# Kernel tuning notes

Hardware: AMD Instinct MI355X
Metric: run time of the kernel (lower is better)

Reference implementation:

```python
import jax, jax.numpy as jnp
import numpy as np

IN_SIZE = 171
HIDDEN = 1024
OUT_SIZE = 171
BATCH = 64
SEQ_LEN = 100
COND_NUM = 5
GT_NUM = 5


def _lstm_cell(x, h, c, w_ih, w_hh, b_ih, b_hh):
    # PyTorch LSTMCell: gates ordered (i, f, g, o)
    gates = x @ w_ih.T + h @ w_hh.T + b_ih + b_hh  # [B, 4H]
    i, f, g, o = jnp.split(gates, 4, axis=-1)
    i = jax.nn.sigmoid(i)
    f = jax.nn.sigmoid(f)
    g = jnp.tanh(g)
    o = jax.nn.sigmoid(o)
    c_new = f * c + i * g
    h_new = o * jnp.tanh(c_new)
    return h_new, c_new


def setup_inputs() -> dict:
    key = jax.random.key(0)
    ks = jax.random.split(key, 15)
    s = 1.0 / np.sqrt(HIDDEN)
    p = {}
    p["real_seq"] = jax.random.normal(ks[0], (BATCH, SEQ_LEN, IN_SIZE), dtype=jnp.float32)
    p["w_ih1"] = jax.random.uniform(ks[1], (4 * HIDDEN, IN_SIZE), minval=-s, maxval=s, dtype=jnp.float32)
    p["w_hh1"] = jax.random.uniform(ks[2], (4 * HIDDEN, HIDDEN), minval=-s, maxval=s, dtype=jnp.float32)
    p["b_ih1"] = jax.random.uniform(ks[3], (4 * HIDDEN,), minval=-s, maxval=s, dtype=jnp.float32)
    p["b_hh1"] = jax.random.uniform(ks[4], (4 * HIDDEN,), minval=-s, maxval=s, dtype=jnp.float32)
    p["w_ih2"] = jax.random.uniform(ks[5], (4 * HIDDEN, HIDDEN), minval=-s, maxval=s, dtype=jnp.float32)
    p["w_hh2"] = jax.random.uniform(ks[6], (4 * HIDDEN, HIDDEN), minval=-s, maxval=s, dtype=jnp.float32)
    p["b_ih2"] = jax.random.uniform(ks[7], (4 * HIDDEN,), minval=-s, maxval=s, dtype=jnp.float32)
    p["b_hh2"] = jax.random.uniform(ks[8], (4 * HIDDEN,), minval=-s, maxval=s, dtype=jnp.float32)
    p["w_ih3"] = jax.random.uniform(ks[9], (4 * HIDDEN, HIDDEN), minval=-s, maxval=s, dtype=jnp.float32)
    p["w_hh3"] = jax.random.uniform(ks[10], (4 * HIDDEN, HIDDEN), minval=-s, maxval=s, dtype=jnp.float32)
    p["b_ih3"] = jax.random.uniform(ks[11], (4 * HIDDEN,), minval=-s, maxval=s, dtype=jnp.float32)
    p["b_hh3"] = jax.random.uniform(ks[12], (4 * HIDDEN,), minval=-s, maxval=s, dtype=jnp.float32)
    p["dec_w"] = jax.random.uniform(ks[13], (OUT_SIZE, HIDDEN), minval=-s, maxval=s, dtype=jnp.float32)
    p["dec_b"] = jax.random.uniform(ks[14], (OUT_SIZE,), minval=-s, maxval=s, dtype=jnp.float32)
    return p


def _condition_lst(seq_len):
    gt = np.ones((100, GT_NUM))
    cond = np.zeros((100, COND_NUM))
    return np.concatenate((gt, cond), axis=1).reshape(-1)[:seq_len]


def reference(real_seq, w_ih1, w_hh1, b_ih1, b_hh1, w_ih2, w_hh2, b_ih2, b_hh2,
              w_ih3, w_hh3, b_ih3, b_hh3, dec_w, dec_b):
    batch, seq_len, _ = real_seq.shape
    cond = jnp.asarray(_condition_lst(seq_len), dtype=real_seq.dtype)  # [T], static pattern
    frames = jnp.swapaxes(real_seq, 0, 1)  # [T, B, in]
    z = jnp.zeros((batch, HIDDEN), dtype=real_seq.dtype)
    out0 = jnp.zeros((batch, OUT_SIZE), dtype=real_seq.dtype)

    def step(carry, xs):
        (h0, c0, h1, c1, h2, c2, prev_out) = carry
        frame, c = xs
        in_frame = jnp.where(c == 1, frame, prev_out)
        h0, c0 = _lstm_cell(in_frame, h0, c0, w_ih1, w_hh1, b_ih1, b_hh1)
        h1, c1 = _lstm_cell(h0, h1, c1, w_ih2, w_hh2, b_ih2, b_hh2)
        h2, c2 = _lstm_cell(h1, h2, c2, w_ih3, w_hh3, b_ih3, b_hh3)
        out = h2 @ dec_w.T + dec_b
        return (h0, c0, h1, c1, h2, c2, out), out

    _, outs = jax.lax.scan(step, (z, z, z, z, z, z, out0), (frames, cond))  # outs [T, B, out]
    # torch concatenates along dim=1 -> [B, T*out]
    return jnp.swapaxes(outs, 0, 1).reshape(batch, seq_len * OUT_SIZE)
```

## Files before the change

### kernel.cpp

```cpp
#include <hip/hip_runtime.h>
#include <hip/hip_fp16.h>


typedef unsigned short u16;
typedef unsigned int u32;
typedef _Float16 f16;
typedef _Float16 h8 __attribute__((ext_vector_type(8)));
typedef float f4 __attribute__((ext_vector_type(4)));
typedef u32 u32x4 __attribute__((ext_vector_type(4)));
typedef u32 u32x2 __attribute__((ext_vector_type(2)));

#define HSZ 65536
#define SENT 0xFFFFFFFFu

static __device__ __forceinline__ f4 mfma16(h8 a, h8 b, f4 c) {
  return __builtin_amdgcn_mfma_f32_16x16x32_f16(a, b, c, 0, 0, 0);
}

static __device__ __forceinline__ float fsig(float x) {
  return 1.f / (1.f + __expf(-x));
}
static __device__ __forceinline__ float ftanh(float x) {
  return 1.f - 2.f / (1.f + __expf(2.f * x));
}

static __device__ __forceinline__ u32 sentmax(h8 v) {
  union { h8 h; u32x4 u; } cv; cv.h = v;
  u32 a = cv.u.x > cv.u.y ? cv.u.x : cv.u.y;
  u32 b = cv.u.z > cv.u.w ? cv.u.z : cv.u.w;
  return a > b ? a : b;
}

static __device__ __forceinline__ h8 bypass_load(const u16* p) {
  u32x4 v;
  asm volatile("global_load_dwordx4 %0, %1, off sc0 sc1"
               : "=v"(v) : "v"(p) : "memory");
  union { u32x4 u; h8 h; } cv; cv.u = v;
  return cv.h;
}

static __device__ __forceinline__ void vm_drain_fence() {
  __builtin_amdgcn_s_waitcnt(0x0f70);
  __builtin_amdgcn_sched_barrier(0);
}

struct P {
  const u16 *w1h, *weff, *w1x, *w2, *w3, *wdec, *fr;
  const float *br, *ba, *b2s, *b3s, *dec_b;
  u16 *h0, *h1, *h2;
  float* out;
};

template<int NJ>
static __device__ __forceinline__ void gemm_hreg(f4* acc, const u16* __restrict__ h,
                                                 const h8 (&wr)[NJ], int kq, int bt2,
                                                 int q, int c) {
  h8 a[NJ * 2];
#pragma unroll
  for (int jj = 0; jj < NJ; ++jj) {
    const u16* hp = h + (size_t)((kq * 8 + jj) * 4 + q) * 512;
#pragma unroll
    for (int t = 0; t < 2; ++t)
      a[jj * 2 + t] = *(const h8*)(hp + ((bt2 * 2 + t) * 16 + c) * 8);
  }
  u32 mx = 0;
#pragma unroll
  for (int i = 0; i < NJ * 2; ++i) { u32 s = sentmax(a[i]); mx = mx > s ? mx : s; }
  if (__builtin_expect(__any((int)(mx == SENT)), 0)) {
    for (;;) {
#pragma unroll
      for (int jj = 0; jj < NJ; ++jj) {
        const u16* hp = h + (size_t)((kq * 8 + jj) * 4 + q) * 512;
#pragma unroll
        for (int t = 0; t < 2; ++t)
          a[jj * 2 + t] = bypass_load(hp + ((bt2 * 2 + t) * 16 + c) * 8);
      }
      vm_drain_fence();
      mx = 0;
#pragma unroll
      for (int i = 0; i < NJ * 2; ++i) { u32 s = sentmax(a[i]); mx = mx > s ? mx : s; }
      if (!__any((int)(mx == SENT))) break;
    }
  }
#pragma unroll
  for (int jj = 0; jj < NJ; ++jj)
#pragma unroll
    for (int t = 0; t < 2; ++t)
      acc[t] = mfma16(a[jj * 2 + t], wr[jj], acc[t]);
}

static __device__ __forceinline__ void gemm_hlds(f4* acc, const u16* __restrict__ h,
                                                 const u16* lw, int ktbase, int kq,
                                                 int bt2, int q, int c, int lane) {
  h8 a[16];
#pragma unroll
  for (int jj = 0; jj < 8; ++jj) {
    const u16* hp = h + (size_t)((kq * 8 + jj) * 4 + q) * 512;
#pragma unroll
    for (int t = 0; t < 2; ++t)
      a[jj * 2 + t] = *(const h8*)(hp + ((bt2 * 2 + t) * 16 + c) * 8);
  }
  u32 mx = 0;
#pragma unroll
  for (int i = 0; i < 16; ++i) { u32 s = sentmax(a[i]); mx = mx > s ? mx : s; }
  if (__builtin_expect(__any((int)(mx == SENT)), 0)) {
    for (;;) {
#pragma unroll
      for (int jj = 0; jj < 8; ++jj) {
        const u16* hp = h + (size_t)((kq * 8 + jj) * 4 + q) * 512;
#pragma unroll
        for (int t = 0; t < 2; ++t)
          a[jj * 2 + t] = bypass_load(hp + ((bt2 * 2 + t) * 16 + c) * 8);
      }
      vm_drain_fence();
      mx = 0;
#pragma unroll
      for (int i = 0; i < 16; ++i) { u32 s = sentmax(a[i]); mx = mx > s ? mx : s; }
      if (!__any((int)(mx == SENT))) break;
    }
  }
#pragma unroll
  for (int jj = 0; jj < 8; ++jj) {
    h8 b = *(const h8*)(lw + (size_t)((ktbase + kq * 8 + jj) * 64 + lane) * 8);
    acc[0] = mfma16(a[jj * 2 + 0], b, acc[0]);
    acc[1] = mfma16(a[jj * 2 + 1], b, acc[1]);
  }
}

static __device__ __forceinline__ void gemm_fr(f4* acc, const u16* __restrict__ frt,
                                               const h8 (&wr)[2], int kq, int bt2,
                                               int q, int c) {
  if (kq < 3) {
#pragma unroll
    for (int jj = 0; jj < 2; ++jj) {
      int kt = kq * 2 + jj;
      h8 b = wr[jj];
#pragma unroll
      for (int t = 0; t < 2; ++t) {
        h8 a = *(const h8*)(frt + (size_t)((bt2 * 2 + t) * 16 + c) * 192 + kt * 32 + q * 8);
        acc[t] = mfma16(a, b, acc[t]);
      }
    }
  }
}

__launch_bounds__(512, 2)
__global__ void lstm_main(P p) {
  const int ng = blockIdx.x;
  const int tid = threadIdx.x;
  const int lane = tid & 63;
  const int w = tid >> 6;
  const int kq = w & 3;
  const int bt2 = w >> 2;
  const int c = lane & 15;
  const int q = lane >> 4;

  __shared__ u16 lds_w2[64 * 512];
  __shared__ u16 lds_w3[64 * 512];
  __shared__ float part[4 * 64 * 17];
  __shared__ float decp[8][64];

  {
    const uint4* s2 = (const uint4*)(p.w2 + (size_t)ng * 64 * 512);
    const uint4* s3 = (const uint4*)(p.w3 + (size_t)ng * 64 * 512);
    uint4* d2 = (uint4*)lds_w2;
    uint4* d3 = (uint4*)lds_w3;
    for (int i = tid; i < 4096; i += 512) { d2[i] = s2[i]; d3[i] = s3[i]; }
  }

  h8 r_w1h[8], r_weff[8], r_w1x[2];
  {
#pragma unroll
    for (int jj = 0; jj < 8; ++jj) {
      r_w1h[jj] = *(const h8*)(p.w1h + (size_t)((ng * 32 + kq * 8 + jj) * 64 + lane) * 8);
      r_weff[jj] = *(const h8*)(p.weff + (size_t)((ng * 32 + kq * 8 + jj) * 64 + lane) * 8);
    }
    if (kq < 3) {
#pragma unroll
      for (int jj = 0; jj < 2; ++jj)
        r_w1x[jj] = *(const h8*)(p.w1x + (size_t)((ng * 6 + kq * 2 + jj) * 64 + lane) * 8);
    }
  }

  float rb_r[16], rb_a[16], rb2[16], rb3[16];
  if (w == 0) {
#pragma unroll
    for (int i = 0; i < 16; ++i) {
      int idx = (i >> 2) * 1024 + ng * 4 + (i & 3);
      rb_r[i] = p.br[idx];  rb_a[i] = p.ba[idx];
      rb2[i] = p.b2s[idx];  rb3[i] = p.b3s[idx];
    }
  }
  const float dec_bng = (ng < 171) ? p.dec_b[ng] : 0.f;
  __syncthreads();

  float cr0[4] = {0, 0, 0, 0}, cr1[4] = {0, 0, 0, 0}, cr2[4] = {0, 0, 0, 0};

  auto combine_pub = [&](float* crL, const float* rb, u16* hw) {
    __builtin_amdgcn_s_setprio(1);
    u32 pk0 = 0, pk1 = 0;
#pragma unroll
    for (int u = 0; u < 4; ++u) {
      float s0 = rb[0 + u], s1 = rb[4 + u], s2 = rb[8 + u], s3 = rb[12 + u];
#pragma unroll
      for (int kqi = 0; kqi < 4; ++kqi) {
        const float* pp = &part[(kqi * 64 + lane) * 17 + u];
        s0 += pp[0]; s1 += pp[4]; s2 += pp[8]; s3 += pp[12];
      }
      float iv = fsig(s0), fv = fsig(s1), gv = ftanh(s2), ov = fsig(s3);
      float cn = fv * crL[u] + iv * gv;
      crL[u] = cn;
      f16 hh = (f16)(ov * ftanh(cn));
      u32 bits = (u32)*(const u16*)&hh;
      if (u < 2) pk0 |= bits << (16 * u); else pk1 |= bits << (16 * (u - 2));
    }
    u32* dst = (u32*)hw + (size_t)(ng >> 1) * 256 + lane * 4 + (ng & 1) * 2;
    u32x2 pk; pk.x = pk0; pk.y = pk1;
    asm volatile("global_store_dwordx2 %0, %1, off sc0 sc1"
                 : : "v"(dst), "v"(pk) : "memory");
    __builtin_amdgcn_s_setprio(0);
  };

  auto canary_wait = [&](const u16* slot) {
    if (w == 1) {
      const u32* cp = (const u32*)slot + (size_t)lane * 512;
      for (;;) {
        u32x4 v0, v1;
        asm volatile("global_load_dwordx4 %0, %2, off sc0 sc1\n\t"
                     "global_load_dwordx4 %1, %3, off sc0 sc1"
                     : "=v"(v0), "=v"(v1) : "v"(cp), "v"(cp + 256) : "memory");
        vm_drain_fence();
        u32 a0 = v0.x > v0.y ? v0.x : v0.y;
        u32 a1 = v0.z > v0.w ? v0.z : v0.w;
        u32 a2 = v1.x > v1.y ? v1.x : v1.y;
        u32 a3 = v1.z > v1.w ? v1.z : v1.w;
        u32 m01 = a0 > a1 ? a0 : a1;
        u32 m23 = a2 > a3 ? a2 : a3;
        u32 m = m01 > m23 ? m01 : m23;
        if (__all((int)(m != SENT))) break;
      }
    }
    __syncthreads();
  };

  auto put_part = [&](const f4* acc) {
#pragma unroll
    for (int t = 0; t < 2; ++t)
#pragma unroll
      for (int r = 0; r < 4; ++r)
        part[(kq * 64 + bt2 * 32 + t * 16 + q * 4 + r) * 17 + c] = acc[t][r];
  };

  auto dec_partial = [&](const u16* __restrict__ h2b) {
    if (ng < 171) {
      const u16* hp = h2b + (size_t)w * 16 * 512 + lane * 8;
      const u16* wp = p.wdec + (size_t)ng * 1024 + w * 128;
      h8 hv[16];
#pragma unroll
      for (int i = 0; i < 16; ++i) hv[i] = *(const h8*)(hp + (size_t)i * 512);
      u32 mx = 0;
#pragma unroll
      for (int i = 0; i < 16; ++i) { u32 s = sentmax(hv[i]); mx = mx > s ? mx : s; }
      if (__builtin_expect(__any((int)(mx == SENT)), 0)) {
        for (;;) {
#pragma unroll
          for (int i = 0; i < 16; ++i) hv[i] = bypass_load(hp + (size_t)i * 512);
          vm_drain_fence();
          mx = 0;
#pragma unroll
          for (int i = 0; i < 16; ++i) { u32 s = sentmax(hv[i]); mx = mx > s ? mx : s; }
          if (!__any((int)(mx == SENT))) break;
        }
      }
      float s = 0.f;
#pragma unroll
      for (int i = 0; i < 16; ++i) {
        h8 wv8 = *(const h8*)(wp + i * 8);
#pragma unroll
        for (int jj = 0; jj < 8; ++jj) s += (float)hv[i][jj] * (float)wv8[jj];
      }
      decp[w][lane] = s;
    }
  };
  auto dec_reduce = [&](int tout) {
    if (ng < 171) {
      float o = dec_bng;
#pragma unroll
      for (int i = 0; i < 8; ++i) o += decp[i][lane];
      p.out[(size_t)lane * 17100 + (size_t)tout * 171 + ng] = o;
    }
  };

  for (int t = 0; t < 100; ++t) {
    const bool cond = (t % 10) < 5;
    const bool hoisted = cond && (t > 0);
    const u16* h0r = p.h0 + (size_t)t * HSZ;
    const u16* h1r = p.h1 + (size_t)t * HSZ;
    const u16* h2r = p.h2 + (size_t)t * HSZ;
    u16* h0w = p.h0 + (size_t)(t + 1) * HSZ;
    u16* h1w = p.h1 + (size_t)(t + 1) * HSZ;
    u16* h2w = p.h2 + (size_t)(t + 1) * HSZ;

    if (!hoisted) {
      f4 acc[2] = {{0, 0, 0, 0}, {0, 0, 0, 0}};
      gemm_hreg<8>(acc, h0r, r_w1h, kq, bt2, q, c);
      if (cond) {
        gemm_fr(acc, p.fr + (size_t)t * 64 * 192, r_w1x, kq, bt2, q, c);
        __syncthreads();
      } else {
        canary_wait(h2r);
        gemm_hreg<8>(acc, h2r, r_weff, kq, bt2, q, c);
      }
      put_part(acc);
      __syncthreads();
      if (w == 0) combine_pub(cr0, cond ? rb_r : rb_a, h0w);
    }
    {
      f4 acc[2] = {{0, 0, 0, 0}, {0, 0, 0, 0}};
      gemm_hlds(acc, h1r, lds_w2, 32, kq, bt2, q, c, lane);
      canary_wait(h0w);
      gemm_hlds(acc, h0w, lds_w2, 0, kq, bt2, q, c, lane);
      put_part(acc);
      __syncthreads();
      if (w == 0) combine_pub(cr1, rb2, h1w);
      if ((t + 1 < 100) && (((t + 1) % 10) < 5)) {
        f4 accA[2] = {{0, 0, 0, 0}, {0, 0, 0, 0}};
        gemm_hreg<8>(accA, h0w, r_w1h, kq, bt2, q, c);
        gemm_fr(accA, p.fr + (size_t)(t + 1) * 64 * 192, r_w1x, kq, bt2, q, c);
        __syncthreads();
        put_part(accA);
        __syncthreads();
        if (w == 0) combine_pub(cr0, rb_r, p.h0 + (size_t)(t + 2) * HSZ);
      }
    }
    {
      f4 acc[2] = {{0, 0, 0, 0}, {0, 0, 0, 0}};
      gemm_hlds(acc, h2r, lds_w3, 32, kq, bt2, q, c, lane);
      if (t > 0) dec_partial(h2r);
      canary_wait(h1w);
      gemm_hlds(acc, h1w, lds_w3, 0, kq, bt2, q, c, lane);
      put_part(acc);
      __syncthreads();
      if (w == 0) combine_pub(cr2, rb3, h2w);
      else if (w == 1 && t > 0) dec_reduce(t - 1);
    }
  }
  canary_wait(p.h2 + (size_t)100 * HSZ);
  dec_partial(p.h2 + (size_t)100 * HSZ);
  __syncthreads();
  if (w == 0) dec_reduce(99);
}


__global__ void pack_w_kernel(const float* __restrict__ srcA, int KA,
                              const float* __restrict__ srcB, int KB,
                              u16* __restrict__ dst, int nkt) {
  int blk = blockIdx.x;
  int ng = blk / nkt, kt = blk % nkt;
  int lane = threadIdx.x;
  int c = lane & 15, q = lane >> 4;
  int row = (c >> 2) * 1024 + ng * 4 + (c & 3);
  int k0 = kt * 32 + q * 8;
  alignas(16) u16 outv[8];
  for (int j = 0; j < 8; ++j) {
    int k = k0 + j;
    float v = 0.f;
    if (k < KA) v = srcA[(size_t)row * KA + k];
    else if (k - KA < KB) v = srcB[(size_t)row * KB + (k - KA)];
    f16 hv = (f16)v;
    outv[j] = *(u16*)&hv;
  }
  *(uint4*)(dst + ((size_t)blk * 64 + lane) * 8) = *(const uint4*)outv;
}

__global__ void pack_weff_kernel(const float* __restrict__ w_ih1,
                                 const float* __restrict__ dec_w, u16* __restrict__ dst) {
  int blk = blockIdx.x;
  int ng = blk >> 5, kt = blk & 31;
  int lane = threadIdx.x;
  int c = lane & 15, q = lane >> 4;
  int row = (c >> 2) * 1024 + ng * 4 + (c & 3);
  int k0 = kt * 32 + q * 8;
  float acc[8] = {0.f, 0.f, 0.f, 0.f, 0.f, 0.f, 0.f, 0.f};
  for (int r = 0; r < 171; ++r) {
    float wi = w_ih1[(size_t)row * 171 + r];
    const float* dw = dec_w + (size_t)r * 1024 + k0;
#pragma unroll
    for (int j = 0; j < 8; ++j) acc[j] += wi * dw[j];
  }
  alignas(16) u16 outv[8];
  for (int j = 0; j < 8; ++j) { f16 hv = (f16)acc[j]; outv[j] = *(u16*)&hv; }
  *(uint4*)(dst + ((size_t)blk * 64 + lane) * 8) = *(const uint4*)outv;
}

__global__ void prep_bias_kernel(const float* b_ih1, const float* b_hh1,
                                 const float* w_ih1, const float* dec_b,
                                 const float* b_ih2, const float* b_hh2,
                                 const float* b_ih3, const float* b_hh3,
                                 float* br, float* ba, float* b2, float* b3) {
  int n = blockIdx.x * 256 + threadIdx.x;
  float s = b_ih1[n] + b_hh1[n];
  br[n] = s;
  float a = 0.f;
  for (int r = 0; r < 171; ++r) a += w_ih1[(size_t)n * 171 + r] * dec_b[r];
  ba[n] = s + a;
  b2[n] = b_ih2[n] + b_hh2[n];
  b3[n] = b_ih3[n] + b_hh3[n];
}

__global__ void pack_frames_kernel(const float* __restrict__ rs, u16* __restrict__ fr) {
  int i = blockIdx.x * 256 + threadIdx.x;
  int j = i % 192;
  int tb = i / 192;
  int b = tb % 64, t = tb / 64;
  float v = (j < 171) ? rs[((size_t)b * 100 + t) * 171 + j] : 0.f;
  f16 hv = (f16)v;
  fr[i] = *(u16*)&hv;
}

__global__ void pack_wdec_kernel(const float* __restrict__ dw, u16* __restrict__ dst) {
  int i = blockIdx.x * 256 + threadIdx.x;
  if (i < 171 * 1024) { f16 hv = (f16)dw[i]; dst[i] = *(u16*)&hv; }
}

__global__ void init_kernel(u32* h0, u32* h1, u32* h2) {
  int i = blockIdx.x * 256 + threadIdx.x;
  const int SLOT = 32768;
  u32 v = (i < SLOT) ? 0u : SENT;
  h0[i] = v; h1[i] = v; h2[i] = v;
}

extern "C" void kernel_launch(void* const* d_in, const int* in_sizes, int n_in,
                              void* d_out, int out_size, void* d_ws, size_t ws_size,
                              hipStream_t stream) {
  const float* real_seq = (const float*)d_in[0];
  const float* w_ih1 = (const float*)d_in[1];
  const float* w_hh1 = (const float*)d_in[2];
  const float* b_ih1 = (const float*)d_in[3];
  const float* b_hh1 = (const float*)d_in[4];
  const float* w_ih2 = (const float*)d_in[5];
  const float* w_hh2 = (const float*)d_in[6];
  const float* b_ih2 = (const float*)d_in[7];
  const float* b_hh2 = (const float*)d_in[8];
  const float* w_ih3 = (const float*)d_in[9];
  const float* w_hh3 = (const float*)d_in[10];
  const float* b_ih3 = (const float*)d_in[11];
  const float* b_hh3 = (const float*)d_in[12];
  const float* dec_w = (const float*)d_in[13];
  const float* dec_b = (const float*)d_in[14];

  char* ws = (char*)d_ws;
  size_t off = 0;
  auto alloc = [&](size_t bytes) {
    char* pp = ws + off;
    off += (bytes + 255) & ~(size_t)255;
    return pp;
  };
  u16* w1h  = (u16*)alloc(256ULL * 32 * 512 * 2);
  u16* weff = (u16*)alloc(256ULL * 32 * 512 * 2);
  u16* w1x  = (u16*)alloc(256ULL * 6 * 512 * 2);
  u16* w2   = (u16*)alloc(256ULL * 64 * 512 * 2);
  u16* w3   = (u16*)alloc(256ULL * 64 * 512 * 2);
  u16* wdec = (u16*)alloc(171ULL * 1024 * 2);
  u16* fr   = (u16*)alloc(100ULL * 64 * 192 * 2);
  u16* h0   = (u16*)alloc(101ULL * HSZ * 2);
  u16* h1   = (u16*)alloc(101ULL * HSZ * 2);
  u16* h2   = (u16*)alloc(101ULL * HSZ * 2);
  float* br  = (float*)alloc(4096 * 4);
  float* ba  = (float*)alloc(4096 * 4);
  float* b2s = (float*)alloc(4096 * 4);
  float* b3s = (float*)alloc(4096 * 4);
  (void)ws_size; (void)in_sizes; (void)n_in; (void)out_size;

  pack_w_kernel<<<256 * 32, 64, 0, stream>>>(w_hh1, 1024, nullptr, 0, w1h, 32);
  pack_w_kernel<<<256 * 6, 64, 0, stream>>>(w_ih1, 171, nullptr, 0, w1x, 6);
  pack_w_kernel<<<256 * 64, 64, 0, stream>>>(w_ih2, 1024, w_hh2, 1024, w2, 64);
  pack_w_kernel<<<256 * 64, 64, 0, stream>>>(w_ih3, 1024, w_hh3, 1024, w3, 64);
  pack_weff_kernel<<<256 * 32, 64, 0, stream>>>(w_ih1, dec_w, weff);
  pack_wdec_kernel<<<(171 * 1024 + 255) / 256, 256, 0, stream>>>(dec_w, wdec);
  pack_frames_kernel<<<100 * 64 * 192 / 256, 256, 0, stream>>>(real_seq, fr);
  prep_bias_kernel<<<16, 256, 0, stream>>>(b_ih1, b_hh1, w_ih1, dec_b,
                                           b_ih2, b_hh2, b_ih3, b_hh3, br, ba, b2s, b3s);
  init_kernel<<<101 * 32768 / 256, 256, 0, stream>>>((u32*)h0, (u32*)h1, (u32*)h2);

  P p{w1h, weff, w1x, w2, w3, wdec, fr, br, ba, b2s, b3s, dec_b,
      h0, h1, h2, (float*)d_out};
  lstm_main<<<256, 512, 0, stream>>>(p);
}
```

Baseline: 1.689 ms.

## Replace single-wave canary polling with per-wave prefetched canary checks

The old wait had one wave poll the sentinel values of the incoming hidden state and then release the block with a barrier. Now every wave issues its own canary load for just the slice it will consume before starting the independent GEMM half, then checks it afterwards. The poll latency is hidden behind compute and the barrier is removed from the dependency wait path. It adds a barrier before put_part, and correctness now depends on each wave's canary slice fully covering the data that wave reads.

```diff
diff --git a/kernel.cpp b/kernel.cpp
--- a/kernel.cpp
+++ b/kernel.cpp
@@ -37,6 +37,13 @@
                : "=v"(v) : "v"(p) : "memory");
   union { u32x4 u; h8 h; } cv; cv.u = v;
   return cv.h;
+}
+
+static __device__ __forceinline__ u32x2 bypass_load8(const u32* p) {
+  u32x2 v;
+  asm volatile("global_load_dwordx2 %0, %1, off sc0 sc1"
+               : "=v"(v) : "v"(p) : "memory");
+  return v;
 }
 
 static __device__ __forceinline__ void vm_drain_fence() {
@@ -221,26 +228,20 @@
     __builtin_amdgcn_s_setprio(0);
   };
 
-  auto canary_wait = [&](const u16* slot) {
-    if (w == 1) {
-      const u32* cp = (const u32*)slot + (size_t)lane * 512;
-      for (;;) {
-        u32x4 v0, v1;
-        asm volatile("global_load_dwordx4 %0, %2, off sc0 sc1\n\t"
-                     "global_load_dwordx4 %1, %3, off sc0 sc1"
-                     : "=v"(v0), "=v"(v1) : "v"(cp), "v"(cp + 256) : "memory");
-        vm_drain_fence();
-        u32 a0 = v0.x > v0.y ? v0.x : v0.y;
-        u32 a1 = v0.z > v0.w ? v0.z : v0.w;
-        u32 a2 = v1.x > v1.y ? v1.x : v1.y;
-        u32 a3 = v1.z > v1.w ? v1.z : v1.w;
-        u32 m01 = a0 > a1 ? a0 : a1;
-        u32 m23 = a2 > a3 ? a2 : a3;
-        u32 m = m01 > m23 ? m01 : m23;
-        if (__all((int)(m != SENT))) break;
-      }
-    }
-    __syncthreads();
+  auto canq_issue = [&](const u16* slot) -> u32x2 {
+    const u32* cp = (const u32*)slot +
+                    (size_t)(kq * 32 + (lane >> 1)) * 256 + (lane & 1) * 2;
+    return bypass_load8(cp);
+  };
+  auto canq_wait = [&](const u16* slot, u32x2 v) {
+    const u32* cp = (const u32*)slot +
+                    (size_t)(kq * 32 + (lane >> 1)) * 256 + (lane & 1) * 2;
+    for (;;) {
+      u32 m = v.x > v.y ? v.x : v.y;
+      if (__all((int)(m != SENT))) break;
+      v = bypass_load8(cp);
+      vm_drain_fence();
+    }
   };
 
   auto put_part = [&](const f4* acc) {
@@ -288,6 +289,17 @@
 #pragma unroll
       for (int i = 0; i < 8; ++i) o += decp[i][lane];
       p.out[(size_t)lane * 17100 + (size_t)tout * 171 + ng] = o;
+    }
+  };
+
+  auto dec_wait = [&](const u16* slot) {
+    const u32* cp = (const u32*)slot +
+                    (size_t)(w * 16 + (lane & 15)) * 256 + ((lane >> 4) & 1) * 2;
+    for (;;) {
+      u32x2 v = bypass_load8(cp);
+      vm_drain_fence();
+      u32 m = v.x > v.y ? v.x : v.y;
+      if (__all((int)(m != SENT))) break;
     }
   };
 
@@ -303,23 +315,32 @@
 
     if (!hoisted) {
       f4 acc[2] = {{0, 0, 0, 0}, {0, 0, 0, 0}};
-      gemm_hreg<8>(acc, h0r, r_w1h, kq, bt2, q, c);
       if (cond) {
+        gemm_hreg<8>(acc, h0r, r_w1h, kq, bt2, q, c);
         gemm_fr(acc, p.fr + (size_t)t * 64 * 192, r_w1x, kq, bt2, q, c);
-        __syncthreads();
       } else {
-        canary_wait(h2r);
+        u32x2 cv = canq_issue(h2r);
+        gemm_hreg<8>(acc, h0r, r_w1h, kq, bt2, q, c);
+        vm_drain_fence();
+        canq_wait(h2r, cv);
         gemm_hreg<8>(acc, h2r, r_weff, kq, bt2, q, c);
       }
+      __syncthreads();
       put_part(acc);
       __syncthreads();
       if (w == 0) combine_pub(cr0, cond ? rb_r : rb_a, h0w);
     }
     {
       f4 acc[2] = {{0, 0, 0, 0}, {0, 0, 0, 0}};
+      u32x2 cv = {0, 0};
+      if (!hoisted) cv = canq_issue(h0w);
       gemm_hlds(acc, h1r, lds_w2, 32, kq, bt2, q, c, lane);
-      canary_wait(h0w);
+      if (!hoisted) {
+        vm_drain_fence();
+        canq_wait(h0w, cv);
+      }
       gemm_hlds(acc, h0w, lds_w2, 0, kq, bt2, q, c, lane);
+      __syncthreads();
       put_part(acc);
       __syncthreads();
       if (w == 0) combine_pub(cr1, rb2, h1w);
@@ -335,17 +356,20 @@
     }
     {
       f4 acc[2] = {{0, 0, 0, 0}, {0, 0, 0, 0}};
+      u32x2 cv = canq_issue(h1w);
       gemm_hlds(acc, h2r, lds_w3, 32, kq, bt2, q, c, lane);
       if (t > 0) dec_partial(h2r);
-      canary_wait(h1w);
+      vm_drain_fence();
+      canq_wait(h1w, cv);
       gemm_hlds(acc, h1w, lds_w3, 0, kq, bt2, q, c, lane);
+      __syncthreads();
       put_part(acc);
       __syncthreads();
       if (w == 0) combine_pub(cr2, rb3, h2w);
       else if (w == 1 && t > 0) dec_reduce(t - 1);
     }
   }
-  canary_wait(p.h2 + (size_t)100 * HSZ);
+  dec_wait(p.h2 + (size_t)100 * HSZ);
   dec_partial(p.h2 + (size_t)100 * HSZ);
   __syncthreads();
   if (w == 0) dec_reduce(99);
```

Measured after the change: 1.860 ms. +10.1%, slower.

## Split LSTM gate combine across two waves and prefetch canary polls before GEMMs

Applied to the files above, without the earlier changes.

The gate-combine/publish step that wave 0 used to do alone over 4 hidden units is now shared by waves 0 and 1, two units each, with one dword store apiece. This shortens the serial tail on the critical path between layers. The readiness (canary) poll moves to wave 7 and is split into issue and finish phases. The first load is issued before the independent half of the GEMM so its latency overlaps the compute, and the decoder reduce moves to wave 2. The cost is more waves in the combine phase and extra registers held across the GEMMs for the prefetched values.

```diff
diff --git a/kernel.cpp b/kernel.cpp
--- a/kernel.cpp
+++ b/kernel.cpp
@@ -182,11 +182,11 @@
     }
   }
 
-  float rb_r[16], rb_a[16], rb2[16], rb3[16];
-  if (w == 0) {
-#pragma unroll
-    for (int i = 0; i < 16; ++i) {
-      int idx = (i >> 2) * 1024 + ng * 4 + (i & 3);
+  float rb_r[8], rb_a[8], rb2[8], rb3[8];
+  if (w < 2) {
+#pragma unroll
+    for (int i = 0; i < 8; ++i) {
+      int idx = (i >> 1) * 1024 + ng * 4 + w * 2 + (i & 1);
       rb_r[i] = p.br[idx];  rb_a[i] = p.ba[idx];
       rb2[i] = p.b2s[idx];  rb3[i] = p.b3s[idx];
     }
@@ -194,41 +194,44 @@
   const float dec_bng = (ng < 171) ? p.dec_b[ng] : 0.f;
   __syncthreads();
 
-  float cr0[4] = {0, 0, 0, 0}, cr1[4] = {0, 0, 0, 0}, cr2[4] = {0, 0, 0, 0};
+  float cr0[2] = {0, 0}, cr1[2] = {0, 0}, cr2[2] = {0, 0};
 
   auto combine_pub = [&](float* crL, const float* rb, u16* hw) {
     __builtin_amdgcn_s_setprio(1);
-    u32 pk0 = 0, pk1 = 0;
-#pragma unroll
-    for (int u = 0; u < 4; ++u) {
-      float s0 = rb[0 + u], s1 = rb[4 + u], s2 = rb[8 + u], s3 = rb[12 + u];
+    u32 pk = 0;
+#pragma unroll
+    for (int lu = 0; lu < 2; ++lu) {
+      int u = (w << 1) + lu;
+      float s0 = rb[0 + lu], s1 = rb[2 + lu], s2 = rb[4 + lu], s3 = rb[6 + lu];
 #pragma unroll
       for (int kqi = 0; kqi < 4; ++kqi) {
         const float* pp = &part[(kqi * 64 + lane) * 17 + u];
         s0 += pp[0]; s1 += pp[4]; s2 += pp[8]; s3 += pp[12];
       }
       float iv = fsig(s0), fv = fsig(s1), gv = ftanh(s2), ov = fsig(s3);
-      float cn = fv * crL[u] + iv * gv;
-      crL[u] = cn;
+      float cn = fv * crL[lu] + iv * gv;
+      crL[lu] = cn;
       f16 hh = (f16)(ov * ftanh(cn));
-      u32 bits = (u32)*(const u16*)&hh;
-      if (u < 2) pk0 |= bits << (16 * u); else pk1 |= bits << (16 * (u - 2));
-    }
-    u32* dst = (u32*)hw + (size_t)(ng >> 1) * 256 + lane * 4 + (ng & 1) * 2;
-    u32x2 pk; pk.x = pk0; pk.y = pk1;
-    asm volatile("global_store_dwordx2 %0, %1, off sc0 sc1"
+      pk |= ((u32)*(const u16*)&hh) << (16 * lu);
+    }
+    u32* dst = (u32*)hw + (size_t)(ng >> 1) * 256 + lane * 4 + (ng & 1) * 2 + w;
+    asm volatile("global_store_dword %0, %1, off sc0 sc1"
                  : : "v"(dst), "v"(pk) : "memory");
     __builtin_amdgcn_s_setprio(0);
   };
 
-  auto canary_wait = [&](const u16* slot) {
-    if (w == 1) {
+  auto can_issue = [&](const u16* slot, u32x4* v0, u32x4* v1) {
+    if (w == 7) {
+      const u32* cp = (const u32*)slot + (size_t)lane * 512;
+      asm volatile("global_load_dwordx4 %0, %2, off sc0 sc1\n\t"
+                   "global_load_dwordx4 %1, %3, off sc0 sc1"
+                   : "=v"(*v0), "=v"(*v1) : "v"(cp), "v"(cp + 256) : "memory");
+    }
+  };
+  auto can_finish = [&](const u16* slot, u32x4 v0, u32x4 v1) {
+    if (w == 7) {
       const u32* cp = (const u32*)slot + (size_t)lane * 512;
       for (;;) {
-        u32x4 v0, v1;
-        asm volatile("global_load_dwordx4 %0, %2, off sc0 sc1\n\t"
-                     "global_load_dwordx4 %1, %3, off sc0 sc1"
-                     : "=v"(v0), "=v"(v1) : "v"(cp), "v"(cp + 256) : "memory");
         vm_drain_fence();
         u32 a0 = v0.x > v0.y ? v0.x : v0.y;
         u32 a1 = v0.z > v0.w ? v0.z : v0.w;
@@ -238,6 +241,9 @@
         u32 m23 = a2 > a3 ? a2 : a3;
         u32 m = m01 > m23 ? m01 : m23;
         if (__all((int)(m != SENT))) break;
+        asm volatile("global_load_dwordx4 %0, %2, off sc0 sc1\n\t"
+                     "global_load_dwordx4 %1, %3, off sc0 sc1"
+                     : "=v"(v0), "=v"(v1) : "v"(cp), "v"(cp + 256) : "memory");
       }
     }
     __syncthreads();
@@ -303,26 +309,31 @@
 
     if (!hoisted) {
       f4 acc[2] = {{0, 0, 0, 0}, {0, 0, 0, 0}};
-      gemm_hreg<8>(acc, h0r, r_w1h, kq, bt2, q, c);
       if (cond) {
+        gemm_hreg<8>(acc, h0r, r_w1h, kq, bt2, q, c);
         gemm_fr(acc, p.fr + (size_t)t * 64 * 192, r_w1x, kq, bt2, q, c);
         __syncthreads();
       } else {
-        canary_wait(h2r);
+        u32x4 cv0 = {0, 0, 0, 0}, cv1 = {0, 0, 0, 0};
+        can_issue(h2r, &cv0, &cv1);
+        gemm_hreg<8>(acc, h0r, r_w1h, kq, bt2, q, c);
+        can_finish(h2r, cv0, cv1);
         gemm_hreg<8>(acc, h2r, r_weff, kq, bt2, q, c);
       }
       put_part(acc);
       __syncthreads();
-      if (w == 0) combine_pub(cr0, cond ? rb_r : rb_a, h0w);
+      if (w < 2) combine_pub(cr0, cond ? rb_r : rb_a, h0w);
     }
     {
       f4 acc[2] = {{0, 0, 0, 0}, {0, 0, 0, 0}};
+      u32x4 cv0 = {0, 0, 0, 0}, cv1 = {0, 0, 0, 0};
+      can_issue(h0w, &cv0, &cv1);
       gemm_hlds(acc, h1r, lds_w2, 32, kq, bt2, q, c, lane);
-      canary_wait(h0w);
+      can_finish(h0w, cv0, cv1);
       gemm_hlds(acc, h0w, lds_w2, 0, kq, bt2, q, c, lane);
       put_part(acc);
       __syncthreads();
-      if (w == 0) combine_pub(cr1, rb2, h1w);
+      if (w < 2) combine_pub(cr1, rb2, h1w);
       if ((t + 1 < 100) && (((t + 1) % 10) < 5)) {
         f4 accA[2] = {{0, 0, 0, 0}, {0, 0, 0, 0}};
         gemm_hreg<8>(accA, h0w, r_w1h, kq, bt2, q, c);
@@ -330,25 +341,31 @@
         __syncthreads();
         put_part(accA);
         __syncthreads();
-        if (w == 0) combine_pub(cr0, rb_r, p.h0 + (size_t)(t + 2) * HSZ);
+        if (w < 2) combine_pub(cr0, rb_r, p.h0 + (size_t)(t + 2) * HSZ);
       }
     }
     {
       f4 acc[2] = {{0, 0, 0, 0}, {0, 0, 0, 0}};
+      u32x4 cv0 = {0, 0, 0, 0}, cv1 = {0, 0, 0, 0};
+      can_issue(h1w, &cv0, &cv1);
       gemm_hlds(acc, h2r, lds_w3, 32, kq, bt2, q, c, lane);
       if (t > 0) dec_partial(h2r);
-      canary_wait(h1w);
+      can_finish(h1w, cv0, cv1);
       gemm_hlds(acc, h1w, lds_w3, 0, kq, bt2, q, c, lane);
       put_part(acc);
       __syncthreads();
-      if (w == 0) combine_pub(cr2, rb3, h2w);
-      else if (w == 1 && t > 0) dec_reduce(t - 1);
-    }
-  }
-  canary_wait(p.h2 + (size_t)100 * HSZ);
-  dec_partial(p.h2 + (size_t)100 * HSZ);
-  __syncthreads();
-  if (w == 0) dec_reduce(99);
+      if (w < 2) combine_pub(cr2, rb3, h2w);
+      else if (w == 2 && t > 0) dec_reduce(t - 1);
+    }
+  }
+  {
+    u32x4 cv0 = {0, 0, 0, 0}, cv1 = {0, 0, 0, 0};
+    can_issue(p.h2 + (size_t)100 * HSZ, &cv0, &cv1);
+    can_finish(p.h2 + (size_t)100 * HSZ, cv0, cv1);
+    dec_partial(p.h2 + (size_t)100 * HSZ);
+    __syncthreads();
+    if (w == 0) dec_reduce(99);
+  }
 }
 
 
```

Measured after the change: 1.825 ms. 8.0% more time.

## Replace sentinel canary polling with per-step flag arrays and early flag prefetch

Applied to the files above, without the earlier changes.

Inter-block readiness is now signalled through a dedicated array of per-block flags, one per publish sequence, instead of polling the hidden-state buffers for sentinel values. Each publishing wave writes its flag after its h store. The waiting wave issues the flag load before the preceding independent GEMM, so the poll latency can overlap useful work. This shrinks polling traffic to one 16-byte load per lane and removes the max-reduction over data. The cost is that readiness no longer checks the data itself: lane 0's flag store is not explicitly ordered after the other lanes' data stores, which could let a consumer read stale h.

```diff
diff --git a/kernel.cpp b/kernel.cpp
--- a/kernel.cpp
+++ b/kernel.cpp
@@ -12,6 +12,7 @@
 
 #define HSZ 65536
 #define SENT 0xFFFFFFFFu
+#define NSEQ 320
 
 static __device__ __forceinline__ f4 mfma16(h8 a, h8 b, f4 c) {
   return __builtin_amdgcn_mfma_f32_16x16x32_f16(a, b, c, 0, 0, 0);
@@ -48,6 +49,7 @@
   const u16 *w1h, *weff, *w1x, *w2, *w3, *wdec, *fr;
   const float *br, *ba, *b2s, *b3s, *dec_b;
   u16 *h0, *h1, *h2;
+  u32* flg;
   float* out;
 };
 
@@ -196,7 +198,7 @@
 
   float cr0[4] = {0, 0, 0, 0}, cr1[4] = {0, 0, 0, 0}, cr2[4] = {0, 0, 0, 0};
 
-  auto combine_pub = [&](float* crL, const float* rb, u16* hw) {
+  auto combine_pub = [&](float* crL, const float* rb, u16* hw, int seqv) {
     __builtin_amdgcn_s_setprio(1);
     u32 pk0 = 0, pk1 = 0;
 #pragma unroll
@@ -218,26 +220,33 @@
     u32x2 pk; pk.x = pk0; pk.y = pk1;
     asm volatile("global_store_dwordx2 %0, %1, off sc0 sc1"
                  : : "v"(dst), "v"(pk) : "memory");
+    if (lane == 0) {
+      u32* fp = p.flg + (size_t)seqv * 256 + ng;
+      u32 one = 1;
+      asm volatile("global_store_dword %0, %1, off sc0 sc1"
+                   : : "v"(fp), "v"(one) : "memory");
+    }
     __builtin_amdgcn_s_setprio(0);
   };
 
-  auto canary_wait = [&](const u16* slot) {
+  auto flag_issue = [&](int seqv, u32x4* v) {
     if (w == 1) {
-      const u32* cp = (const u32*)slot + (size_t)lane * 512;
+      const u32* fp = p.flg + (size_t)seqv * 256 + lane * 4;
+      asm volatile("global_load_dwordx4 %0, %1, off sc0 sc1"
+                   : "=v"(*v) : "v"(fp) : "memory");
+    }
+  };
+  auto flag_finish = [&](int seqv, u32x4 v) {
+    if (w == 1) {
+      const u32* fp = p.flg + (size_t)seqv * 256 + lane * 4;
       for (;;) {
-        u32x4 v0, v1;
-        asm volatile("global_load_dwordx4 %0, %2, off sc0 sc1\n\t"
-                     "global_load_dwordx4 %1, %3, off sc0 sc1"
-                     : "=v"(v0), "=v"(v1) : "v"(cp), "v"(cp + 256) : "memory");
         vm_drain_fence();
-        u32 a0 = v0.x > v0.y ? v0.x : v0.y;
-        u32 a1 = v0.z > v0.w ? v0.z : v0.w;
-        u32 a2 = v1.x > v1.y ? v1.x : v1.y;
-        u32 a3 = v1.z > v1.w ? v1.z : v1.w;
-        u32 m01 = a0 > a1 ? a0 : a1;
-        u32 m23 = a2 > a3 ? a2 : a3;
-        u32 m = m01 > m23 ? m01 : m23;
-        if (__all((int)(m != SENT))) break;
+        u32 m01 = v.x < v.y ? v.x : v.y;
+        u32 m23 = v.z < v.w ? v.z : v.w;
+        u32 mn = m01 < m23 ? m01 : m23;
+        if (__all((int)(mn != 0))) break;
+        asm volatile("global_load_dwordx4 %0, %1, off sc0 sc1"
+                     : "=v"(v) : "v"(fp) : "memory");
       }
     }
     __syncthreads();
@@ -291,9 +300,12 @@
     }
   };
 
+  int seq = 0, seqA = 0, seqB = 0, seqC = 0;
+
   for (int t = 0; t < 100; ++t) {
     const bool cond = (t % 10) < 5;
     const bool hoisted = cond && (t > 0);
+    const bool hoistNext = (t + 1 < 100) && (((t + 1) % 10) < 5);
     const u16* h0r = p.h0 + (size_t)t * HSZ;
     const u16* h1r = p.h1 + (size_t)t * HSZ;
     const u16* h2r = p.h2 + (size_t)t * HSZ;
@@ -303,52 +315,67 @@
 
     if (!hoisted) {
       f4 acc[2] = {{0, 0, 0, 0}, {0, 0, 0, 0}};
-      gemm_hreg<8>(acc, h0r, r_w1h, kq, bt2, q, c);
       if (cond) {
+        gemm_hreg<8>(acc, h0r, r_w1h, kq, bt2, q, c);
         gemm_fr(acc, p.fr + (size_t)t * 64 * 192, r_w1x, kq, bt2, q, c);
         __syncthreads();
       } else {
-        canary_wait(h2r);
+        u32x4 fv = {0, 0, 0, 0};
+        flag_issue(seqC, &fv);
+        gemm_hreg<8>(acc, h0r, r_w1h, kq, bt2, q, c);
+        flag_finish(seqC, fv);
         gemm_hreg<8>(acc, h2r, r_weff, kq, bt2, q, c);
       }
       put_part(acc);
       __syncthreads();
-      if (w == 0) combine_pub(cr0, cond ? rb_r : rb_a, h0w);
+      seqA = seq++;
+      if (w == 0) combine_pub(cr0, cond ? rb_r : rb_a, h0w, seqA);
     }
     {
       f4 acc[2] = {{0, 0, 0, 0}, {0, 0, 0, 0}};
+      u32x4 fv = {0, 0, 0, 0};
+      flag_issue(seqA, &fv);
       gemm_hlds(acc, h1r, lds_w2, 32, kq, bt2, q, c, lane);
-      canary_wait(h0w);
+      flag_finish(seqA, fv);
       gemm_hlds(acc, h0w, lds_w2, 0, kq, bt2, q, c, lane);
       put_part(acc);
       __syncthreads();
-      if (w == 0) combine_pub(cr1, rb2, h1w);
-      if ((t + 1 < 100) && (((t + 1) % 10) < 5)) {
+      seqB = seq++;
+      if (w == 0) combine_pub(cr1, rb2, h1w, seqB);
+      if (hoistNext) {
         f4 accA[2] = {{0, 0, 0, 0}, {0, 0, 0, 0}};
         gemm_hreg<8>(accA, h0w, r_w1h, kq, bt2, q, c);
         gemm_fr(accA, p.fr + (size_t)(t + 1) * 64 * 192, r_w1x, kq, bt2, q, c);
         __syncthreads();
         put_part(accA);
         __syncthreads();
-        if (w == 0) combine_pub(cr0, rb_r, p.h0 + (size_t)(t + 2) * HSZ);
+        seqA = seq++;
+        if (w == 0) combine_pub(cr0, rb_r, p.h0 + (size_t)(t + 2) * HSZ, seqA);
       }
     }
     {
       f4 acc[2] = {{0, 0, 0, 0}, {0, 0, 0, 0}};
+      u32x4 fv = {0, 0, 0, 0};
+      flag_issue(seqB, &fv);
       gemm_hlds(acc, h2r, lds_w3, 32, kq, bt2, q, c, lane);
       if (t > 0) dec_partial(h2r);
-      canary_wait(h1w);
+      flag_finish(seqB, fv);
       gemm_hlds(acc, h1w, lds_w3, 0, kq, bt2, q, c, lane);
       put_part(acc);
       __syncthreads();
-      if (w == 0) combine_pub(cr2, rb3, h2w);
+      seqC = seq++;
+      if (w == 0) combine_pub(cr2, rb3, h2w, seqC);
       else if (w == 1 && t > 0) dec_reduce(t - 1);
     }
   }
-  canary_wait(p.h2 + (size_t)100 * HSZ);
-  dec_partial(p.h2 + (size_t)100 * HSZ);
-  __syncthreads();
-  if (w == 0) dec_reduce(99);
+  {
+    u32x4 fv = {0, 0, 0, 0};
+    flag_issue(seqC, &fv);
+    flag_finish(seqC, fv);
+    dec_partial(p.h2 + (size_t)100 * HSZ);
+    __syncthreads();
+    if (w == 0) dec_reduce(99);
+  }
 }
 
 
@@ -423,11 +450,12 @@
   if (i < 171 * 1024) { f16 hv = (f16)dw[i]; dst[i] = *(u16*)&hv; }
 }
 
-__global__ void init_kernel(u32* h0, u32* h1, u32* h2) {
+__global__ void init_kernel(u32* h0, u32* h1, u32* h2, u32* flg) {
   int i = blockIdx.x * 256 + threadIdx.x;
   const int SLOT = 32768;
   u32 v = (i < SLOT) ? 0u : SENT;
   h0[i] = v; h1[i] = v; h2[i] = v;
+  if (i < NSEQ * 256) flg[i] = 0;
 }
 
 extern "C" void kernel_launch(void* const* d_in, const int* in_sizes, int n_in,
@@ -470,6 +498,7 @@
   float* ba  = (float*)alloc(4096 * 4);
   float* b2s = (float*)alloc(4096 * 4);
   float* b3s = (float*)alloc(4096 * 4);
+  u32* flg   = (u32*)alloc((size_t)NSEQ * 256 * 4);
   (void)ws_size; (void)in_sizes; (void)n_in; (void)out_size;
 
   pack_w_kernel<<<256 * 32, 64, 0, stream>>>(w_hh1, 1024, nullptr, 0, w1h, 32);
@@ -481,9 +510,9 @@
   pack_frames_kernel<<<100 * 64 * 192 / 256, 256, 0, stream>>>(real_seq, fr);
   prep_bias_kernel<<<16, 256, 0, stream>>>(b_ih1, b_hh1, w_ih1, dec_b,
                                            b_ih2, b_hh2, b_ih3, b_hh3, br, ba, b2s, b3s);
-  init_kernel<<<101 * 32768 / 256, 256, 0, stream>>>((u32*)h0, (u32*)h1, (u32*)h2);
+  init_kernel<<<101 * 32768 / 256, 256, 0, stream>>>((u32*)h0, (u32*)h1, (u32*)h2, flg);
 
   P p{w1h, weff, w1x, w2, w3, wdec, fr, br, ba, b2s, b3s, dec_b,
-      h0, h1, h2, (float*)d_out};
+      h0, h1, h2, flg, (float*)d_out};
   lstm_main<<<256, 512, 0, stream>>>(p);
 }
```

Result: slower. 2.102 ms (+24.4%).
